# Performance work log

Hardware: AMD Instinct MI355X
Metric: run time of the kernel (lower is better)

## Reference

```python
import jax, jax.numpy as jnp
import numpy as np

B, Q, D, H, P, F = 16, 300, 256, 8, 4, 2048
HG = WG = 100          # feature-map height/width (hw = 10000, perfect square)
HW = HG * WG
DH = D // H
EPS = 1e-5


def _ln(x, g, b):
    m = x.mean(-1, keepdims=True)
    v = jnp.var(x, axis=-1, keepdims=True)
    return (x - m) * jax.lax.rsqrt(v + EPS) * g + b


def setup_inputs() -> dict:
    key = jax.random.key(0)
    ks = jax.random.split(key, 24)
    rn = lambda k, shape, s=0.02: jax.random.normal(k, shape, jnp.float32) * s
    return {
        "tgt": jax.random.normal(ks[0], (B, Q, D), jnp.float32),
        "memory": jax.random.normal(ks[1], (B, HW, D), jnp.float32),
        "in_proj_w": rn(ks[2], (D, 3 * D)), "in_proj_b": rn(ks[3], (3 * D,)),
        "out_proj_w": rn(ks[4], (D, D)), "out_proj_b": rn(ks[5], (D,)),
        "norm1_g": jnp.ones((D,), jnp.float32), "norm1_b": jnp.zeros((D,), jnp.float32),
        "ref_w": rn(ks[6], (D, 2)), "ref_b": rn(ks[7], (2,)),
        "off_w": rn(ks[8], (D, H * P * 2)), "off_b": rn(ks[9], (H * P * 2,)),
        "attw_w": rn(ks[10], (D, H * P)), "attw_b": rn(ks[11], (H * P,)),
        "vproj_w": rn(ks[12], (D, D)), "vproj_b": rn(ks[13], (D,)),
        "oproj_w": rn(ks[14], (D, D)), "oproj_b": rn(ks[15], (D,)),
        "norm2_g": jnp.ones((D,), jnp.float32), "norm2_b": jnp.zeros((D,), jnp.float32),
        "lin1_w": rn(ks[16], (D, F)), "lin1_b": rn(ks[17], (F,)),
        "lin2_w": rn(ks[18], (F, D)), "lin2_b": rn(ks[19], (D,)),
        "norm3_g": jnp.ones((D,), jnp.float32), "norm3_b": jnp.zeros((D,), jnp.float32),
    }


def reference(tgt, memory, in_proj_w, in_proj_b, out_proj_w, out_proj_b,
              norm1_g, norm1_b, ref_w, ref_b, off_w, off_b, attw_w, attw_b,
              vproj_w, vproj_b, oproj_w, oproj_b, norm2_g, norm2_b,
              lin1_w, lin1_b, lin2_w, lin2_b, norm3_g, norm3_b):
    # ---- self-attention (nn.MultiheadAttention, eval mode: dropout = identity)
    qkv = tgt @ in_proj_w + in_proj_b                      # [B,Q,3D]
    q, k, v = jnp.split(qkv, 3, axis=-1)
    q = q.reshape(B, Q, H, DH)
    k = k.reshape(B, Q, H, DH)
    v = v.reshape(B, Q, H, DH)
    scores = jnp.einsum('bqhd,bkhd->bhqk', q, k) / jnp.sqrt(jnp.float32(DH))
    attn = jax.nn.softmax(scores, axis=-1)
    sa = jnp.einsum('bhqk,bkhd->bqhd', attn, v).reshape(B, Q, D) @ out_proj_w + out_proj_b
    x = _ln(tgt + sa, norm1_g, norm1_b)

    # ---- reference points
    ref = jax.nn.sigmoid(x @ ref_w + ref_b)                # [B,Q,2] in (0,1)

    # ---- deformable cross-attention
    offs = (x @ off_w + off_b).reshape(B, Q, H, P, 2)
    wts = jax.nn.softmax((x @ attw_w + attw_b).reshape(B, Q, H, P), axis=-1)
    vals = (memory @ vproj_w + vproj_b).reshape(B, HW, H, DH)
    loc = jnp.clip(ref[:, :, None, None, :] + offs, 0.0, 1.0)
    sx = loc[..., 0] * (WG - 1)
    sy = loc[..., 1] * (HG - 1)
    x0 = jnp.floor(sx)
    y0 = jnp.floor(sy)
    x0i = jnp.clip(x0.astype(jnp.int32), 0, WG - 1)
    y0i = jnp.clip(y0.astype(jnp.int32), 0, HG - 1)
    x1i = jnp.clip(x0i + 1, 0, WG - 1)
    y1i = jnp.clip(y0i + 1, 0, HG - 1)
    wx1 = sx - x0
    wx0 = 1.0 - wx1
    wy1 = sy - y0
    wy0 = 1.0 - wy1
    bi = jnp.arange(B)[:, None, None, None]
    hi = jnp.arange(H)[None, None, :, None]

    def gather(yi, xi):                                    # [B,Q,H,P,DH]
        return vals[bi, yi * WG + xi, hi]

    samp = (gather(y0i, x0i) * (wx0 * wy0)[..., None]
            + gather(y1i, x0i) * (wx0 * wy1)[..., None]
            + gather(y0i, x1i) * (wx1 * wy0)[..., None]
            + gather(y1i, x1i) * (wx1 * wy1)[..., None])
    ca = (samp * wts[..., None]).sum(axis=3).reshape(B, Q, D) @ oproj_w + oproj_b
    x = _ln(x + ca, norm2_g, norm2_b)

    # ---- FFN
    ff = jax.nn.relu(x @ lin1_w + lin1_b) @ lin2_w + lin2_b
    return _ln(x + ff, norm3_g, norm3_b)
```

## Files before the change

### kernel.cpp

```cpp
#include <hip/hip_runtime.h>

#define NB   16
#define NQ   300
#define ND   256
#define NH   8
#define NP   4
#define NF   2048
#define NHW  10000
#define NWG  100
#define NROW 4800

typedef __attribute__((ext_vector_type(8))) short bf16x8;
typedef __attribute__((ext_vector_type(4))) float f32x4;

__device__ __forceinline__ unsigned short f2bf(float f) {
    unsigned u = __builtin_bit_cast(unsigned, f);
    u = (u + 0x7fffu + ((u >> 16) & 1u)) >> 16;
    return (unsigned short)u;
}
__device__ __forceinline__ float bf2f(unsigned short h) {
    unsigned u = ((unsigned)h) << 16;
    return __builtin_bit_cast(float, u);
}

__device__ __forceinline__ void gl_lds16(const unsigned short* g, unsigned short* l) {
    __builtin_amdgcn_global_load_lds(
        (__attribute__((address_space(1))) const void*)g,
        (__attribute__((address_space(3))) void*)l,
        16, 0, 0);
}

__global__ __launch_bounds__(256) void transpose_cast(
    const float* __restrict__ w_in,  const float* __restrict__ w_out,
    const float* __restrict__ w_vp,  const float* __restrict__ w_op,
    const float* __restrict__ w_l1,  const float* __restrict__ w_l2,
    unsigned short* __restrict__ o_in, unsigned short* __restrict__ o_out,
    unsigned short* __restrict__ o_vp, unsigned short* __restrict__ o_op,
    unsigned short* __restrict__ o_l1, unsigned short* __restrict__ o_l2)
{
    __shared__ float ts[64][65];
    int b = blockIdx.x;
    const float* src; unsigned short* dst; int K, N, ncx;
    if      (b < 48)  { src = w_in;  dst = o_in;  K = 256;  N = 768;  ncx = 12; }
    else if (b < 64)  { src = w_out; dst = o_out; K = 256;  N = 256;  ncx = 4;  b -= 48; }
    else if (b < 80)  { src = w_vp;  dst = o_vp;  K = 256;  N = 256;  ncx = 4;  b -= 64; }
    else if (b < 96)  { src = w_op;  dst = o_op;  K = 256;  N = 256;  ncx = 4;  b -= 80; }
    else if (b < 224) { src = w_l1;  dst = o_l1;  K = 256;  N = 2048; ncx = 32; b -= 96; }
    else              { src = w_l2;  dst = o_l2;  K = 2048; N = 256;  ncx = 4;  b -= 224; }
    const int n0 = (b % ncx) * 64, k0 = (b / ncx) * 64;
    const int t = threadIdx.x;
    const int r = t >> 4, c = t & 15;
    #pragma unroll
    for (int j = 0; j < 4; j++) {
        float4 v = *(const float4*)(src + (long)(k0 + j * 16 + r) * N + n0 + c * 4);
        ts[j * 16 + r][c * 4 + 0] = v.x;
        ts[j * 16 + r][c * 4 + 1] = v.y;
        ts[j * 16 + r][c * 4 + 2] = v.z;
        ts[j * 16 + r][c * 4 + 3] = v.w;
    }
    __syncthreads();
    #pragma unroll
    for (int j = 0; j < 4; j++) {
        unsigned short o[4];
        #pragma unroll
        for (int i = 0; i < 4; i++)
            o[i] = f2bf(ts[c * 4 + i][j * 16 + r]);
        *(uint2*)(dst + (long)(n0 + j * 16 + r) * K + k0 + c * 4) = *(uint2*)o;
    }
}

__global__ __launch_bounds__(256) void prep_head(
    const float* __restrict__ rw, const float* __restrict__ rb,
    const float* __restrict__ ow, const float* __restrict__ ob,
    const float* __restrict__ aw, const float* __restrict__ ab,
    unsigned short* __restrict__ o_hd, float* __restrict__ o_hb)
{
    int id = blockIdx.x * 256 + threadIdx.x;
    if (id < 32768) {
        int n = id >> 8, k = id & 255;
        float v;
        if (n < 2)       v = rw[k * 2 + n];
        else if (n < 66) v = ow[k * 64 + (n - 2)];
        else if (n < 98) v = aw[k * 32 + (n - 66)];
        else             v = 0.0f;
        o_hd[id] = f2bf(v);
        return;
    }
    id -= 32768;
    if (id < 128) {
        float v;
        if (id < 2)       v = rb[id];
        else if (id < 66) v = ob[id - 2];
        else if (id < 98) v = ab[id - 66];
        else              v = 0.0f;
        o_hb[id] = v;
    }
}

template <int RELU, int OUTBF, int SPLITK, int TM>
__global__ __launch_bounds__(256, 4) void gemm_bt(
    const float* __restrict__ A, const unsigned short* __restrict__ Bt,
    const float* __restrict__ bias, void* __restrict__ Cout,
    int M, int N, int K)
{
    static_assert(TM == 64, "tile is 64x128");
    __shared__ __align__(16) unsigned short As[2][64 * 32];
    __shared__ __align__(16) unsigned short Bs[2][128 * 32];
    const int t    = threadIdx.x;
    const long m0  = (long)blockIdx.y * 64;
    const int  n0  = blockIdx.x * 128;
    const int  wave = t >> 6, lane = t & 63;
    const int  l16 = lane & 15, quad = lane >> 4;
    const int  wm  = (wave >> 1) << 5;
    const int  wn  = (wave & 1) << 6;
    const int  fA  = (wave >> 1) << 1;
    const int  fB  = (wave & 1) << 2;

    f32x4 acc[2][4] = {};

    const int kChunk = K / SPLITK;
    const int kBeg   = (SPLITK > 1) ? blockIdx.z * kChunk : 0;
    const int nk     = kChunk / 32;

    const float* aP =
        A + (m0 + wave * 16 + l16) * (long)K + kBeg + (quad << 3);
    const unsigned short* bP =
        Bt + (long)(n0 + wave * 32 + l16) * K + kBeg + (quad << 3);
    unsigned short* aW  = &As[0][(wave << 9) + (lane << 3)];
    unsigned short* bW0 = &Bs[0][(wave << 10)];

    float4 fa0, fa1;
    auto loadA = [&](int kt) {
        fa0 = *(const float4*)(aP + kt * 32);
        fa1 = *(const float4*)(aP + kt * 32 + 4);
    };
    auto issueB = [&](int kt, int buf) {
        gl_lds16(bP + kt * 32,          bW0 + buf * 4096);
        gl_lds16(bP + kt * 32 + 16 * K, bW0 + buf * 4096 + 512);
    };
    auto writeA = [&](int buf) {
        unsigned short ta[8] = {f2bf(fa0.x), f2bf(fa0.y), f2bf(fa0.z), f2bf(fa0.w),
                                f2bf(fa1.x), f2bf(fa1.y), f2bf(fa1.z), f2bf(fa1.w)};
        *(uint4*)(aW + buf * 2048) = *(const uint4*)ta;
    };

    loadA(0);
    issueB(0, 0);
    writeA(0);
    __syncthreads();

    for (int kt = 0; kt < nk; kt++) {
        const int cur = kt & 1;
        if (kt + 1 < nk) {
            issueB(kt + 1, cur ^ 1);
            loadA(kt + 1);
        }

        const bf16x8 af0 = *(const bf16x8*)&As[cur][(fA + 0) * 512 + (lane << 3)];
        const bf16x8 af1 = *(const bf16x8*)&As[cur][(fA + 1) * 512 + (lane << 3)];
        #pragma unroll
        for (int j = 0; j < 4; j++) {
            const bf16x8 bv = *(const bf16x8*)&Bs[cur][(fB + j) * 512 + (lane << 3)];
            acc[0][j] = __builtin_amdgcn_mfma_f32_16x16x32_bf16(bv, af0, acc[0][j], 0, 0, 0);
            acc[1][j] = __builtin_amdgcn_mfma_f32_16x16x32_bf16(bv, af1, acc[1][j], 0, 0, 0);
        }

        if (kt + 1 < nk) {
            writeA(cur ^ 1);
            __syncthreads();
        }
    }

    float4 bj[4];
    #pragma unroll
    for (int j = 0; j < 4; j++)
        bj[j] = *(const float4*)&bias[n0 + wn + j * 16 + (quad << 2)];

    float* outp = (float*)Cout;
    float bscale = 1.0f;
    if (SPLITK > 1) {
        outp += (size_t)blockIdx.z * M * N;
        bscale = (blockIdx.z == 0) ? 1.0f : 0.0f;
    }

    #pragma unroll
    for (int i = 0; i < 2; i++) {
        const long gr = m0 + wm + i * 16 + l16;
        #pragma unroll
        for (int j = 0; j < 4; j++) {
            float4 v;
            v.x = acc[i][j][0] + bscale * bj[j].x;
            v.y = acc[i][j][1] + bscale * bj[j].y;
            v.z = acc[i][j][2] + bscale * bj[j].z;
            v.w = acc[i][j][3] + bscale * bj[j].w;
            if (RELU) {
                v.x = fmaxf(v.x, 0.f); v.y = fmaxf(v.y, 0.f);
                v.z = fmaxf(v.z, 0.f); v.w = fmaxf(v.w, 0.f);
            }
            const int gc = n0 + wn + j * 16 + (quad << 2);
            if (OUTBF) {
                unsigned short o[4] = {f2bf(v.x), f2bf(v.y), f2bf(v.z), f2bf(v.w)};
                *(uint2*)((unsigned short*)Cout + gr * N + gc) = *(uint2*)o;
            } else {
                *(float4*)(outp + gr * N + gc) = v;
            }
        }
    }
}

__global__ __launch_bounds__(256) void attn_kernel(
    const float* __restrict__ qkv, float* __restrict__ sa)
{
    __shared__ union {
        struct {
            unsigned short Ks[304][40];
            unsigned short Qs[64][40];
        } s;
        unsigned short Ps[4][16][328];
    } u;
    __shared__ unsigned short Vt[32][328];

    const int bh = blockIdx.y;
    const int b  = bh >> 3, h = bh & 7;
    const int q0 = blockIdx.x * 64;
    const int t  = threadIdx.x;

    for (int idx = t; idx < 304 * 8; idx += 256) {
        const int r = idx >> 3, c4 = (idx & 7) << 2;
        if (r < NQ) {
            const float4 kv = *(const float4*)(qkv + ((long)(b * NQ + r)) * 768 + 256 + h * 32 + c4);
            u.s.Ks[r][c4 + 0] = f2bf(kv.x); u.s.Ks[r][c4 + 1] = f2bf(kv.y);
            u.s.Ks[r][c4 + 2] = f2bf(kv.z); u.s.Ks[r][c4 + 3] = f2bf(kv.w);
        } else {
            u.s.Ks[r][c4 + 0] = 0; u.s.Ks[r][c4 + 1] = 0;
            u.s.Ks[r][c4 + 2] = 0; u.s.Ks[r][c4 + 3] = 0;
        }
    }
    for (int idx = t; idx < NQ * 8; idx += 256) {
        const int key = idx >> 3, dq = (idx & 7) << 2;
        const float4 vv = *(const float4*)(qkv + ((long)(b * NQ + key)) * 768 + 512 + h * 32 + dq);
        Vt[dq + 0][key] = f2bf(vv.x); Vt[dq + 1][key] = f2bf(vv.y);
        Vt[dq + 2][key] = f2bf(vv.z); Vt[dq + 3][key] = f2bf(vv.w);
    }
    for (int idx = t; idx < 32 * 20; idx += 256)
        Vt[idx / 20][300 + idx % 20] = 0;
    for (int idx = t; idx < 64 * 8; idx += 256) {
        const int r = idx >> 3, c4 = (idx & 7) << 2;
        const int q = q0 + r;
        if (q < NQ) {
            const float4 qv = *(const float4*)(qkv + ((long)(b * NQ + q)) * 768 + h * 32 + c4);
            u.s.Qs[r][c4 + 0] = f2bf(qv.x); u.s.Qs[r][c4 + 1] = f2bf(qv.y);
            u.s.Qs[r][c4 + 2] = f2bf(qv.z); u.s.Qs[r][c4 + 3] = f2bf(qv.w);
        } else {
            u.s.Qs[r][c4 + 0] = 0; u.s.Qs[r][c4 + 1] = 0;
            u.s.Qs[r][c4 + 2] = 0; u.s.Qs[r][c4 + 3] = 0;
        }
    }
    __syncthreads();

    const int wave = t >> 6, lane = t & 63;
    const int l16 = lane & 15, quad = lane >> 4;
    const float scale = 0.1767766952966369f;

    const bf16x8 aq = *(const bf16x8*)&u.s.Qs[wave * 16 + l16][quad * 8];
    f32x4 sacc[19];
    #pragma unroll
    for (int kt = 0; kt < 19; kt++) {
        const bf16x8 bk = *(const bf16x8*)&u.s.Ks[kt * 16 + l16][quad * 8];
        sacc[kt] = __builtin_amdgcn_mfma_f32_16x16x32_bf16(
            aq, bk, (f32x4){0.f, 0.f, 0.f, 0.f}, 0, 0, 0);
    }

    float inv[4];
    #pragma unroll
    for (int r = 0; r < 4; r++) {
        float m = -1e30f;
        #pragma unroll
        for (int kt = 0; kt < 19; kt++) {
            float s = sacc[kt][r] * scale;
            if (kt == 18 && l16 >= 12) s = -1e30f;
            sacc[kt][r] = s;
            m = fmaxf(m, s);
        }
        m = fmaxf(m, __shfl_xor(m, 1)); m = fmaxf(m, __shfl_xor(m, 2));
        m = fmaxf(m, __shfl_xor(m, 4)); m = fmaxf(m, __shfl_xor(m, 8));
        float sum = 0.f;
        #pragma unroll
        for (int kt = 0; kt < 19; kt++) {
            float p = __expf(sacc[kt][r] - m);
            sacc[kt][r] = p;
            sum += p;
        }
        sum += __shfl_xor(sum, 1); sum += __shfl_xor(sum, 2);
        sum += __shfl_xor(sum, 4); sum += __shfl_xor(sum, 8);
        inv[r] = 1.0f / sum;
    }

    __syncthreads();

    #pragma unroll
    for (int kt = 0; kt < 19; kt++)
        #pragma unroll
        for (int r = 0; r < 4; r++)
            u.Ps[wave][quad * 4 + r][kt * 16 + l16] = f2bf(sacc[kt][r] * inv[r]);
    #pragma unroll
    for (int r = 0; r < 4; r++)
        u.Ps[wave][quad * 4 + r][304 + l16] = 0;

    f32x4 o0 = {0.f, 0.f, 0.f, 0.f}, o1 = {0.f, 0.f, 0.f, 0.f};
    #pragma unroll
    for (int kt = 0; kt < 10; kt++) {
        const bf16x8 ap  = *(const bf16x8*)&u.Ps[wave][l16][kt * 32 + quad * 8];
        const bf16x8 bv0 = *(const bf16x8*)&Vt[l16][kt * 32 + quad * 8];
        const bf16x8 bv1 = *(const bf16x8*)&Vt[16 + l16][kt * 32 + quad * 8];
        o0 = __builtin_amdgcn_mfma_f32_16x16x32_bf16(ap, bv0, o0, 0, 0, 0);
        o1 = __builtin_amdgcn_mfma_f32_16x16x32_bf16(ap, bv1, o1, 0, 0, 0);
    }

    #pragma unroll
    for (int r = 0; r < 4; r++) {
        const int q = q0 + wave * 16 + quad * 4 + r;
        if (q < NQ) {
            float* op = sa + ((long)(b * NQ + q)) * ND + h * 32;
            op[l16]      = o0[r];
            op[16 + l16] = o1[r];
        }
    }
}

template <int NPART>
__global__ __launch_bounds__(256) void residual_ln(
    const float* __restrict__ a, const float* __restrict__ r,
    const float* __restrict__ gam, const float* __restrict__ bet,
    float* __restrict__ out, long pstride)
{
    const int row  = blockIdx.x * 4 + (threadIdx.x >> 6);
    const int lane = threadIdx.x & 63;
    const long base = (long)row * ND + lane * 4;
    float4 av = *(const float4*)(a + base);
    float4 rv = *(const float4*)(r + base);
    #pragma unroll
    for (int z = 1; z < NPART; z++) {
        float4 pv = *(const float4*)(r + z * pstride + base);
        rv.x += pv.x; rv.y += pv.y; rv.z += pv.z; rv.w += pv.w;
    }
    float x0 = av.x + rv.x, x1 = av.y + rv.y, x2 = av.z + rv.z, x3 = av.w + rv.w;
    float s  = x0 + x1 + x2 + x3;
    float s2 = x0 * x0 + x1 * x1 + x2 * x2 + x3 * x3;
    #pragma unroll
    for (int off = 32; off >= 1; off >>= 1) {
        s  += __shfl_xor(s, off);
        s2 += __shfl_xor(s2, off);
    }
    float mean = s * 0.00390625f;
    float var  = s2 * 0.00390625f - mean * mean;
    float rstd = rsqrtf(var + 1e-5f);
    float4 gv = *(const float4*)(gam + lane * 4);
    float4 bv = *(const float4*)(bet + lane * 4);
    float4 o;
    o.x = (x0 - mean) * rstd * gv.x + bv.x;
    o.y = (x1 - mean) * rstd * gv.y + bv.y;
    o.z = (x2 - mean) * rstd * gv.z + bv.z;
    o.w = (x3 - mean) * rstd * gv.w + bv.w;
    *(float4*)(out + base) = o;
}

__global__ __launch_bounds__(256) void meta_kernel(
    const float* __restrict__ res, float* __restrict__ meta)
{
    const int t   = threadIdx.x;
    const int row = blockIdx.x * 8 + (t >> 5);
    const int s   = t & 31;
    const int h   = s >> 2;
    const float* rp = res + (long)row * 128;
    const float rx = 1.f / (1.f + __expf(-rp[0]));
    const float ry = 1.f / (1.f + __expf(-rp[1]));
    const float offx = rp[2 + 2 * s], offy = rp[3 + 2 * s];
    const float a0 = rp[66 + h * 4 + 0], a1 = rp[66 + h * 4 + 1];
    const float a2 = rp[66 + h * 4 + 2], a3 = rp[66 + h * 4 + 3];
    const float mx = fmaxf(fmaxf(a0, a1), fmaxf(a2, a3));
    const float den = __expf(a0 - mx) + __expf(a1 - mx) +
                      __expf(a2 - mx) + __expf(a3 - mx);
    const float awt = __expf(rp[66 + s] - mx) / den;

    const float lx = fminf(fmaxf(rx + offx, 0.f), 1.f) * (NWG - 1);
    const float ly = fminf(fmaxf(ry + offy, 0.f), 1.f) * (NWG - 1);
    const float fx = floorf(lx), fy = floorf(ly);
    int x0 = (int)fx; x0 = min(max(x0, 0), NWG - 1);
    int y0 = (int)fy; y0 = min(max(y0, 0), NWG - 1);
    const int x1 = min(x0 + 1, NWG - 1);
    const int y1 = min(y0 + 1, NWG - 1);
    const float wx1 = lx - fx, wx0 = 1.f - wx1;
    const float wy1 = ly - fy, wy0 = 1.f - wy1;
    float4 m0, m1;
    m0.x = __int_as_float(y0 * NWG + x0);
    m0.y = __int_as_float(y0 * NWG + x1);
    m0.z = __int_as_float(y1 * NWG + x0);
    m0.w = __int_as_float(y1 * NWG + x1);
    m1.x = awt * wx0 * wy0;
    m1.y = awt * wx1 * wy0;
    m1.z = awt * wx0 * wy1;
    m1.w = awt * wx1 * wy1;
    float* mp = meta + (long)row * 256 + s * 8;
    *(float4*)mp       = m0;
    *(float4*)(mp + 4) = m1;
}

__global__ __launch_bounds__(256) void deform_gather(
    const float* __restrict__ meta, const unsigned short* __restrict__ vals,
    float* __restrict__ ca)
{
    const int row = blockIdx.x;
    const int b = row / NQ;
    __shared__ float ms[256];
    const int t = threadIdx.x;
    ms[t] = meta[(long)row * 256 + t];
    __syncthreads();
    const int h = t >> 5, d = t & 31;
    const unsigned short* vb = vals + (long)b * NHW * ND + h * 32 + d;
    float acc = 0.f;
    #pragma unroll
    for (int p = 0; p < NP; p++) {
        const float* mp = ms + h * 32 + p * 8;
        const int i00 = __float_as_int(mp[0]);
        const int i01 = __float_as_int(mp[1]);
        const int i10 = __float_as_int(mp[2]);
        const int i11 = __float_as_int(mp[3]);
        acc += mp[4] * bf2f(vb[(long)i00 * ND]);
        acc += mp[5] * bf2f(vb[(long)i01 * ND]);
        acc += mp[6] * bf2f(vb[(long)i10 * ND]);
        acc += mp[7] * bf2f(vb[(long)i11 * ND]);
    }
    ca[(long)row * ND + t] = acc;
}

extern "C" void kernel_launch(void* const* d_in, const int* in_sizes, int n_in,
                              void* d_out, int out_size, void* d_ws, size_t ws_size,
                              hipStream_t stream)
{
    (void)in_sizes; (void)n_in; (void)out_size; (void)ws_size;
    const float* tgt   = (const float*)d_in[0];
    const float* mem   = (const float*)d_in[1];
    const float* inpw  = (const float*)d_in[2];
    const float* inpb  = (const float*)d_in[3];
    const float* outw  = (const float*)d_in[4];
    const float* outb  = (const float*)d_in[5];
    const float* n1g   = (const float*)d_in[6];
    const float* n1b   = (const float*)d_in[7];
    const float* refw  = (const float*)d_in[8];
    const float* refb  = (const float*)d_in[9];
    const float* offw  = (const float*)d_in[10];
    const float* offb  = (const float*)d_in[11];
    const float* attww = (const float*)d_in[12];
    const float* attwb = (const float*)d_in[13];
    const float* vpw   = (const float*)d_in[14];
    const float* vpb   = (const float*)d_in[15];
    const float* opw   = (const float*)d_in[16];
    const float* opb   = (const float*)d_in[17];
    const float* n2g   = (const float*)d_in[18];
    const float* n2b   = (const float*)d_in[19];
    const float* l1w   = (const float*)d_in[20];
    const float* l1b   = (const float*)d_in[21];
    const float* l2w   = (const float*)d_in[22];
    const float* l2b   = (const float*)d_in[23];
    const float* n3g   = (const float*)d_in[24];
    const float* n3b   = (const float*)d_in[25];
    float* out = (float*)d_out;

    char* p = (char*)d_ws;
    auto alloc = [&](size_t bytes) {
        char* r = p; p += (bytes + 255) & ~(size_t)255; return (void*)r;
    };
    unsigned short* wtIn   = (unsigned short*)alloc(768 * 256 * 2);
    unsigned short* wtOut  = (unsigned short*)alloc(256 * 256 * 2);
    unsigned short* wtVp   = (unsigned short*)alloc(256 * 256 * 2);
    unsigned short* wtOp   = (unsigned short*)alloc(256 * 256 * 2);
    unsigned short* wtL1   = (unsigned short*)alloc(2048 * 256 * 2);
    unsigned short* wtL2   = (unsigned short*)alloc(256 * 2048 * 2);
    unsigned short* wtHead = (unsigned short*)alloc(128 * 256 * 2);
    float*          headb  = (float*)alloc(128 * 4);
    float* qkv  = (float*)alloc((size_t)NROW * 768 * 4);
    float* sa   = (float*)alloc((size_t)NROW * ND * 4);
    float* x1   = (float*)alloc((size_t)NROW * ND * 4);
    float* x2   = (float*)alloc((size_t)NROW * ND * 4);
    float* tmp  = (float*)alloc((size_t)NROW * ND * 4 * 4);
    float* ca   = (float*)alloc((size_t)NROW * ND * 4);
    float* meta = (float*)alloc((size_t)NROW * 256 * 4);
    void* uni = alloc((size_t)NB * NHW * ND * 2);
    unsigned short* vals = (unsigned short*)uni;
    float* h1 = (float*)uni;
    float* res = qkv;

    transpose_cast<<<352, 256, 0, stream>>>(
        inpw, outw, vpw, opw, l1w, l2w,
        wtIn, wtOut, wtVp, wtOp, wtL1, wtL2);
    prep_head<<<129, 256, 0, stream>>>(refw, refb, offw, offb, attww, attwb,
                                       wtHead, headb);

    gemm_bt<0, 0, 1, 64><<<dim3(6, 75), 256, 0, stream>>>(tgt, wtIn, inpb, qkv,
                                                          NROW, 768, 256);
    gemm_bt<0, 1, 1, 64><<<dim3(2, 2500), 256, 0, stream>>>(mem, wtVp, vpb, vals,
                                                            NB * NHW, 256, 256);
    attn_kernel<<<dim3(5, 128), 256, 0, stream>>>(qkv, sa);
    gemm_bt<0, 0, 1, 64><<<dim3(2, 75), 256, 0, stream>>>(sa, wtOut, outb, tmp,
                                                          NROW, 256, 256);
    residual_ln<1><<<1200, 256, 0, stream>>>(tgt, tmp, n1g, n1b, x1, 0);
    gemm_bt<0, 0, 1, 64><<<dim3(1, 75), 256, 0, stream>>>(x1, wtHead, headb, res,
                                                          NROW, 128, 256);
    meta_kernel<<<600, 256, 0, stream>>>(res, meta);
    deform_gather<<<4800, 256, 0, stream>>>(meta, vals, ca);
    gemm_bt<0, 0, 1, 64><<<dim3(2, 75), 256, 0, stream>>>(ca, wtOp, opb, tmp,
                                                          NROW, 256, 256);
    residual_ln<1><<<1200, 256, 0, stream>>>(x1, tmp, n2g, n2b, x2, 0);
    gemm_bt<1, 0, 1, 64><<<dim3(16, 75), 256, 0, stream>>>(x2, wtL1, l1b, h1,
                                                           NROW, 2048, 256);
    gemm_bt<0, 0, 4, 64><<<dim3(2, 75, 4), 256, 0, stream>>>(h1, wtL2, l2b, tmp,
                                                             NROW, 256, 2048);
    residual_ln<4><<<1200, 256, 0, stream>>>(x2, tmp, n3g, n3b, out,
                                             (long)NROW * 256);
}
```

Measured before the change: 514.9 us.

## Drop LDS staging in GEMM; load fragments directly from global into registers

```diff
diff --git a/kernel.cpp b/kernel.cpp
--- a/kernel.cpp
+++ b/kernel.cpp
@@ -23,11 +23,14 @@
     return __builtin_bit_cast(float, u);
 }
 
-__device__ __forceinline__ void gl_lds16(const unsigned short* g, unsigned short* l) {
-    __builtin_amdgcn_global_load_lds(
-        (__attribute__((address_space(1))) const void*)g,
-        (__attribute__((address_space(3))) void*)l,
-        16, 0, 0);
+__device__ __forceinline__ bf16x8 cvt8(float4 lo, float4 hi) {
+    unsigned r0, r1, r2, r3;
+    asm("v_cvt_pk_bf16_f32 %0, %1, %2" : "=v"(r0) : "v"(lo.x), "v"(lo.y));
+    asm("v_cvt_pk_bf16_f32 %0, %1, %2" : "=v"(r1) : "v"(lo.z), "v"(lo.w));
+    asm("v_cvt_pk_bf16_f32 %0, %1, %2" : "=v"(r2) : "v"(hi.x), "v"(hi.y));
+    asm("v_cvt_pk_bf16_f32 %0, %1, %2" : "=v"(r3) : "v"(hi.z), "v"(hi.w));
+    uint4 u = {r0, r1, r2, r3};
+    return __builtin_bit_cast(bf16x8, u);
 }
 
 __global__ __launch_bounds__(256) void transpose_cast(
@@ -97,15 +100,12 @@
     }
 }
 
-template <int RELU, int OUTBF, int SPLITK, int TM>
+template <int RELU, int OUTBF, int SPLITK>
 __global__ __launch_bounds__(256, 4) void gemm_bt(
     const float* __restrict__ A, const unsigned short* __restrict__ Bt,
     const float* __restrict__ bias, void* __restrict__ Cout,
     int M, int N, int K)
 {
-    static_assert(TM == 64, "tile is 64x128");
-    __shared__ __align__(16) unsigned short As[2][64 * 32];
-    __shared__ __align__(16) unsigned short Bs[2][128 * 32];
     const int t    = threadIdx.x;
     const long m0  = (long)blockIdx.y * 64;
     const int  n0  = blockIdx.x * 128;
@@ -113,8 +113,6 @@
     const int  l16 = lane & 15, quad = lane >> 4;
     const int  wm  = (wave >> 1) << 5;
     const int  wn  = (wave & 1) << 6;
-    const int  fA  = (wave >> 1) << 1;
-    const int  fB  = (wave & 1) << 2;
 
     f32x4 acc[2][4] = {};
 
@@ -122,53 +120,45 @@
     const int kBeg   = (SPLITK > 1) ? blockIdx.z * kChunk : 0;
     const int nk     = kChunk / 32;
 
-    const float* aP =
-        A + (m0 + wave * 16 + l16) * (long)K + kBeg + (quad << 3);
-    const unsigned short* bP =
-        Bt + (long)(n0 + wave * 32 + l16) * K + kBeg + (quad << 3);
-    unsigned short* aW  = &As[0][(wave << 9) + (lane << 3)];
-    unsigned short* bW0 = &Bs[0][(wave << 10)];
-
-    float4 fa0, fa1;
-    auto loadA = [&](int kt) {
-        fa0 = *(const float4*)(aP + kt * 32);
-        fa1 = *(const float4*)(aP + kt * 32 + 4);
+    const float* aP0 = A + (m0 + wm + l16) * (long)K + kBeg + (quad << 3);
+    const float* aP1 = aP0 + 16 * (long)K;
+    const unsigned short* bP = Bt + (long)(n0 + wn + l16) * K + kBeg + (quad << 3);
+    const long bStep = 16 * (long)K;
+
+    float4 xa0, xa1, xa2, xa3;
+    float4 ya0, ya1, ya2, ya3;
+
+    auto loadAX = [&](int kt) {
+        const int ko = kt << 5;
+        xa0 = *(const float4*)(aP0 + ko);     xa1 = *(const float4*)(aP0 + ko + 4);
+        xa2 = *(const float4*)(aP1 + ko);     xa3 = *(const float4*)(aP1 + ko + 4);
     };
-    auto issueB = [&](int kt, int buf) {
-        gl_lds16(bP + kt * 32,          bW0 + buf * 4096);
-        gl_lds16(bP + kt * 32 + 16 * K, bW0 + buf * 4096 + 512);
+    auto loadAY = [&](int kt) {
+        const int ko = kt << 5;
+        ya0 = *(const float4*)(aP0 + ko);     ya1 = *(const float4*)(aP0 + ko + 4);
+        ya2 = *(const float4*)(aP1 + ko);     ya3 = *(const float4*)(aP1 + ko + 4);
     };
-    auto writeA = [&](int buf) {
-        unsigned short ta[8] = {f2bf(fa0.x), f2bf(fa0.y), f2bf(fa0.z), f2bf(fa0.w),
-                                f2bf(fa1.x), f2bf(fa1.y), f2bf(fa1.z), f2bf(fa1.w)};
-        *(uint4*)(aW + buf * 2048) = *(const uint4*)ta;
+    auto compute = [&](float4 a0, float4 a1, float4 a2, float4 a3, int kt) {
+        const int ko = kt << 5;
+        bf16x8 bfr[4];
+        #pragma unroll
+        for (int j = 0; j < 4; j++)
+            bfr[j] = *(const bf16x8*)(bP + j * bStep + ko);
+        const bf16x8 af0 = cvt8(a0, a1);
+        const bf16x8 af1 = cvt8(a2, a3);
+        #pragma unroll
+        for (int j = 0; j < 4; j++) {
+            acc[0][j] = __builtin_amdgcn_mfma_f32_16x16x32_bf16(bfr[j], af0, acc[0][j], 0, 0, 0);
+            acc[1][j] = __builtin_amdgcn_mfma_f32_16x16x32_bf16(bfr[j], af1, acc[1][j], 0, 0, 0);
+        }
     };
 
-    loadA(0);
-    issueB(0, 0);
-    writeA(0);
-    __syncthreads();
-
-    for (int kt = 0; kt < nk; kt++) {
-        const int cur = kt & 1;
-        if (kt + 1 < nk) {
-            issueB(kt + 1, cur ^ 1);
-            loadA(kt + 1);
-        }
-
-        const bf16x8 af0 = *(const bf16x8*)&As[cur][(fA + 0) * 512 + (lane << 3)];
-        const bf16x8 af1 = *(const bf16x8*)&As[cur][(fA + 1) * 512 + (lane << 3)];
-        #pragma unroll
-        for (int j = 0; j < 4; j++) {
-            const bf16x8 bv = *(const bf16x8*)&Bs[cur][(fB + j) * 512 + (lane << 3)];
-            acc[0][j] = __builtin_amdgcn_mfma_f32_16x16x32_bf16(bv, af0, acc[0][j], 0, 0, 0);
-            acc[1][j] = __builtin_amdgcn_mfma_f32_16x16x32_bf16(bv, af1, acc[1][j], 0, 0, 0);
-        }
-
-        if (kt + 1 < nk) {
-            writeA(cur ^ 1);
-            __syncthreads();
-        }
+    loadAX(0);
+    for (int kt = 0; kt < nk; kt += 2) {
+        loadAY(kt + 1);
+        compute(xa0, xa1, xa2, xa3, kt);
+        if (kt + 2 < nk) loadAX(kt + 2);
+        compute(ya0, ya1, ya2, ya3, kt + 1);
     }
 
     float4 bj[4];
@@ -497,25 +487,25 @@
     prep_head<<<129, 256, 0, stream>>>(refw, refb, offw, offb, attww, attwb,
                                        wtHead, headb);
 
-    gemm_bt<0, 0, 1, 64><<<dim3(6, 75), 256, 0, stream>>>(tgt, wtIn, inpb, qkv,
-                                                          NROW, 768, 256);
-    gemm_bt<0, 1, 1, 64><<<dim3(2, 2500), 256, 0, stream>>>(mem, wtVp, vpb, vals,
-                                                            NB * NHW, 256, 256);
+    gemm_bt<0, 0, 1><<<dim3(6, 75), 256, 0, stream>>>(tgt, wtIn, inpb, qkv,
+                                                      NROW, 768, 256);
+    gemm_bt<0, 1, 1><<<dim3(2, 2500), 256, 0, stream>>>(mem, wtVp, vpb, vals,
+                                                        NB * NHW, 256, 256);
     attn_kernel<<<dim3(5, 128), 256, 0, stream>>>(qkv, sa);
-    gemm_bt<0, 0, 1, 64><<<dim3(2, 75), 256, 0, stream>>>(sa, wtOut, outb, tmp,
-                                                          NROW, 256, 256);
+    gemm_bt<0, 0, 1><<<dim3(2, 75), 256, 0, stream>>>(sa, wtOut, outb, tmp,
+                                                      NROW, 256, 256);
     residual_ln<1><<<1200, 256, 0, stream>>>(tgt, tmp, n1g, n1b, x1, 0);
-    gemm_bt<0, 0, 1, 64><<<dim3(1, 75), 256, 0, stream>>>(x1, wtHead, headb, res,
-                                                          NROW, 128, 256);
+    gemm_bt<0, 0, 1><<<dim3(1, 75), 256, 0, stream>>>(x1, wtHead, headb, res,
+                                                      NROW, 128, 256);
     meta_kernel<<<600, 256, 0, stream>>>(res, meta);
     deform_gather<<<4800, 256, 0, stream>>>(meta, vals, ca);
-    gemm_bt<0, 0, 1, 64><<<dim3(2, 75), 256, 0, stream>>>(ca, wtOp, opb, tmp,
-                                                          NROW, 256, 256);
+    gemm_bt<0, 0, 1><<<dim3(2, 75), 256, 0, stream>>>(ca, wtOp, opb, tmp,
+                                                      NROW, 256, 256);
     residual_ln<1><<<1200, 256, 0, stream>>>(x1, tmp, n2g, n2b, x2, 0);
-    gemm_bt<1, 0, 1, 64><<<dim3(16, 75), 256, 0, stream>>>(x2, wtL1, l1b, h1,
-                                                           NROW, 2048, 256);
-    gemm_bt<0, 0, 4, 64><<<dim3(2, 75, 4), 256, 0, stream>>>(h1, wtL2, l2b, tmp,
-                                                             NROW, 256, 2048);
+    gemm_bt<1, 0, 1><<<dim3(16, 75), 256, 0, stream>>>(x2, wtL1, l1b, h1,
+                                                       NROW, 2048, 256);
+    gemm_bt<0, 0, 4><<<dim3(2, 75, 4), 256, 0, stream>>>(h1, wtL2, l2b, tmp,
+                                                         NROW, 256, 2048);
     residual_ln<4><<<1200, 256, 0, stream>>>(x2, tmp, n3g, n3b, out,
                                              (long)NROW * 256);
 }
```

New measurement: 627.4 us. +21.9%, slower.

## Enlarge GEMM tiles to 128xTN with 512-thread blocks and packed bf16 convert

Applied to the files above, without the earlier changes.

```diff
diff --git a/kernel.cpp b/kernel.cpp
--- a/kernel.cpp
+++ b/kernel.cpp
@@ -21,6 +21,16 @@
 __device__ __forceinline__ float bf2f(unsigned short h) {
     unsigned u = ((unsigned)h) << 16;
     return __builtin_bit_cast(float, u);
+}
+
+__device__ __forceinline__ bf16x8 cvt8(float4 lo, float4 hi) {
+    unsigned r0, r1, r2, r3;
+    asm("v_cvt_pk_bf16_f32 %0, %1, %2" : "=v"(r0) : "v"(lo.x), "v"(lo.y));
+    asm("v_cvt_pk_bf16_f32 %0, %1, %2" : "=v"(r1) : "v"(lo.z), "v"(lo.w));
+    asm("v_cvt_pk_bf16_f32 %0, %1, %2" : "=v"(r2) : "v"(hi.x), "v"(hi.y));
+    asm("v_cvt_pk_bf16_f32 %0, %1, %2" : "=v"(r3) : "v"(hi.z), "v"(hi.w));
+    uint4 u = {r0, r1, r2, r3};
+    return __builtin_bit_cast(bf16x8, u);
 }
 
 __device__ __forceinline__ void gl_lds16(const unsigned short* g, unsigned short* l) {
@@ -97,55 +107,75 @@
     }
 }
 
-template <int RELU, int OUTBF, int SPLITK, int TM>
-__global__ __launch_bounds__(256, 4) void gemm_bt(
+template <int RELU, int OUTBF, int SPLITK, int TN>
+__global__ __launch_bounds__(512, 4) void gemm_bt(
     const float* __restrict__ A, const unsigned short* __restrict__ Bt,
     const float* __restrict__ bias, void* __restrict__ Cout,
     int M, int N, int K)
 {
-    static_assert(TM == 64, "tile is 64x128");
-    __shared__ __align__(16) unsigned short As[2][64 * 32];
-    __shared__ __align__(16) unsigned short Bs[2][128 * 32];
+    constexpr int NFB = TN / 16;
+    constexpr int WN  = TN / 64;
+    constexpr int AI  = WN;
+
+    __shared__ __align__(16) unsigned short As[2][8 * 512];
+    __shared__ __align__(16) unsigned short Bs[2][NFB * 512];
+
     const int t    = threadIdx.x;
-    const long m0  = (long)blockIdx.y * 64;
-    const int  n0  = blockIdx.x * 128;
+    const long m0  = (long)blockIdx.y * 128;
+    const int  n0  = blockIdx.x * TN;
     const int  wave = t >> 6, lane = t & 63;
     const int  l16 = lane & 15, quad = lane >> 4;
-    const int  wm  = (wave >> 1) << 5;
-    const int  wn  = (wave & 1) << 6;
-    const int  fA  = (wave >> 1) << 1;
-    const int  fB  = (wave & 1) << 2;
-
-    f32x4 acc[2][4] = {};
+    const int  wmi = wave / WN, wni = wave % WN;
+    const int  wm  = wmi * (AI * 16);
+    const int  wn  = wni * 64;
+    const int  fA  = wmi * AI;
+    const int  fB  = wni * 4;
+
+    f32x4 acc[AI][4] = {};
 
     const int kChunk = K / SPLITK;
     const int kBeg   = (SPLITK > 1) ? blockIdx.z * kChunk : 0;
     const int nk     = kChunk / 32;
 
-    const float* aP =
-        A + (m0 + wave * 16 + l16) * (long)K + kBeg + (quad << 3);
-    const unsigned short* bP =
-        Bt + (long)(n0 + wave * 32 + l16) * K + kBeg + (quad << 3);
-    unsigned short* aW  = &As[0][(wave << 9) + (lane << 3)];
-    unsigned short* bW0 = &Bs[0][(wave << 10)];
-
-    float4 fa0, fa1;
+    const long aRow   = m0 + wave * 16 + l16;
+    const bool aValid = (aRow < M);
+    const float* aP   = A + aRow * (long)K + kBeg + (quad << 3);
+    unsigned short* aW = &As[0][(wave << 9) + (lane << 3)];
+
+    const unsigned short* bP;
+    unsigned short* bW;
+    if constexpr (TN == 256) {
+        bP = Bt + (long)(n0 + wave * 32 + l16) * K + kBeg + (quad << 3);
+        bW = &Bs[0][wave << 10];
+    } else {
+        bP = Bt + (long)(n0 + wave * 16 + l16) * K + kBeg + (quad << 3);
+        bW = &Bs[0][wave << 9];
+    }
+
+    float4 la0 = make_float4(0.f, 0.f, 0.f, 0.f);
+    float4 la1 = make_float4(0.f, 0.f, 0.f, 0.f);
+
     auto loadA = [&](int kt) {
-        fa0 = *(const float4*)(aP + kt * 32);
-        fa1 = *(const float4*)(aP + kt * 32 + 4);
+        if (aValid) {
+            la0 = *(const float4*)(aP + kt * 32);
+            la1 = *(const float4*)(aP + kt * 32 + 4);
+        }
+    };
+    auto writeA = [&](int buf) {
+        const bf16x8 v = cvt8(la0, la1);
+        *(bf16x8*)(aW + buf * 4096) = v;
     };
     auto issueB = [&](int kt, int buf) {
-        gl_lds16(bP + kt * 32,          bW0 + buf * 4096);
-        gl_lds16(bP + kt * 32 + 16 * K, bW0 + buf * 4096 + 512);
+        if constexpr (TN == 256) {
+            gl_lds16(bP + kt * 32,          bW + buf * (NFB * 512));
+            gl_lds16(bP + kt * 32 + 16 * (long)K, bW + buf * (NFB * 512) + 512);
+        } else {
+            gl_lds16(bP + kt * 32,          bW + buf * (NFB * 512));
+        }
     };
-    auto writeA = [&](int buf) {
-        unsigned short ta[8] = {f2bf(fa0.x), f2bf(fa0.y), f2bf(fa0.z), f2bf(fa0.w),
-                                f2bf(fa1.x), f2bf(fa1.y), f2bf(fa1.z), f2bf(fa1.w)};
-        *(uint4*)(aW + buf * 2048) = *(const uint4*)ta;
-    };
-
+
+    issueB(0, 0);
     loadA(0);
-    issueB(0, 0);
     writeA(0);
     __syncthreads();
 
@@ -156,14 +186,19 @@
             loadA(kt + 1);
         }
 
-        const bf16x8 af0 = *(const bf16x8*)&As[cur][(fA + 0) * 512 + (lane << 3)];
-        const bf16x8 af1 = *(const bf16x8*)&As[cur][(fA + 1) * 512 + (lane << 3)];
-        #pragma unroll
-        for (int j = 0; j < 4; j++) {
-            const bf16x8 bv = *(const bf16x8*)&Bs[cur][(fB + j) * 512 + (lane << 3)];
-            acc[0][j] = __builtin_amdgcn_mfma_f32_16x16x32_bf16(bv, af0, acc[0][j], 0, 0, 0);
-            acc[1][j] = __builtin_amdgcn_mfma_f32_16x16x32_bf16(bv, af1, acc[1][j], 0, 0, 0);
-        }
+        bf16x8 af[AI], bfr[4];
+        #pragma unroll
+        for (int i = 0; i < AI; i++)
+            af[i] = *(const bf16x8*)&As[cur][(fA + i) * 512 + (lane << 3)];
+        #pragma unroll
+        for (int j = 0; j < 4; j++)
+            bfr[j] = *(const bf16x8*)&Bs[cur][(fB + j) * 512 + (lane << 3)];
+        #pragma unroll
+        for (int i = 0; i < AI; i++)
+            #pragma unroll
+            for (int j = 0; j < 4; j++)
+                acc[i][j] = __builtin_amdgcn_mfma_f32_16x16x32_bf16(
+                    bfr[j], af[i], acc[i][j], 0, 0, 0);
 
         if (kt + 1 < nk) {
             writeA(cur ^ 1);
@@ -184,25 +219,27 @@
     }
 
     #pragma unroll
-    for (int i = 0; i < 2; i++) {
+    for (int i = 0; i < AI; i++) {
         const long gr = m0 + wm + i * 16 + l16;
-        #pragma unroll
-        for (int j = 0; j < 4; j++) {
-            float4 v;
-            v.x = acc[i][j][0] + bscale * bj[j].x;
-            v.y = acc[i][j][1] + bscale * bj[j].y;
-            v.z = acc[i][j][2] + bscale * bj[j].z;
-            v.w = acc[i][j][3] + bscale * bj[j].w;
-            if (RELU) {
-                v.x = fmaxf(v.x, 0.f); v.y = fmaxf(v.y, 0.f);
-                v.z = fmaxf(v.z, 0.f); v.w = fmaxf(v.w, 0.f);
-            }
-            const int gc = n0 + wn + j * 16 + (quad << 2);
-            if (OUTBF) {
-                unsigned short o[4] = {f2bf(v.x), f2bf(v.y), f2bf(v.z), f2bf(v.w)};
-                *(uint2*)((unsigned short*)Cout + gr * N + gc) = *(uint2*)o;
-            } else {
-                *(float4*)(outp + gr * N + gc) = v;
+        if (gr < M) {
+            #pragma unroll
+            for (int j = 0; j < 4; j++) {
+                float4 v;
+                v.x = acc[i][j][0] + bscale * bj[j].x;
+                v.y = acc[i][j][1] + bscale * bj[j].y;
+                v.z = acc[i][j][2] + bscale * bj[j].z;
+                v.w = acc[i][j][3] + bscale * bj[j].w;
+                if (RELU) {
+                    v.x = fmaxf(v.x, 0.f); v.y = fmaxf(v.y, 0.f);
+                    v.z = fmaxf(v.z, 0.f); v.w = fmaxf(v.w, 0.f);
+                }
+                const int gc = n0 + wn + j * 16 + (quad << 2);
+                if (OUTBF) {
+                    unsigned short o[4] = {f2bf(v.x), f2bf(v.y), f2bf(v.z), f2bf(v.w)};
+                    *(uint2*)((unsigned short*)Cout + gr * N + gc) = *(uint2*)o;
+                } else {
+                    *(float4*)(outp + gr * N + gc) = v;
+                }
             }
         }
     }
@@ -497,25 +534,25 @@
     prep_head<<<129, 256, 0, stream>>>(refw, refb, offw, offb, attww, attwb,
                                        wtHead, headb);
 
-    gemm_bt<0, 0, 1, 64><<<dim3(6, 75), 256, 0, stream>>>(tgt, wtIn, inpb, qkv,
-                                                          NROW, 768, 256);
-    gemm_bt<0, 1, 1, 64><<<dim3(2, 2500), 256, 0, stream>>>(mem, wtVp, vpb, vals,
-                                                            NB * NHW, 256, 256);
+    gemm_bt<0, 0, 1, 256><<<dim3(3, 38), 512, 0, stream>>>(tgt, wtIn, inpb, qkv,
+                                                           NROW, 768, 256);
+    gemm_bt<0, 1, 1, 256><<<dim3(1, 1250), 512, 0, stream>>>(mem, wtVp, vpb, vals,
+                                                             NB * NHW, 256, 256);
     attn_kernel<<<dim3(5, 128), 256, 0, stream>>>(qkv, sa);
-    gemm_bt<0, 0, 1, 64><<<dim3(2, 75), 256, 0, stream>>>(sa, wtOut, outb, tmp,
-                                                          NROW, 256, 256);
+    gemm_bt<0, 0, 1, 256><<<dim3(1, 38), 512, 0, stream>>>(sa, wtOut, outb, tmp,
+                                                           NROW, 256, 256);
     residual_ln<1><<<1200, 256, 0, stream>>>(tgt, tmp, n1g, n1b, x1, 0);
-    gemm_bt<0, 0, 1, 64><<<dim3(1, 75), 256, 0, stream>>>(x1, wtHead, headb, res,
-                                                          NROW, 128, 256);
+    gemm_bt<0, 0, 1, 128><<<dim3(1, 38), 512, 0, stream>>>(x1, wtHead, headb, res,
+                                                           NROW, 128, 256);
     meta_kernel<<<600, 256, 0, stream>>>(res, meta);
     deform_gather<<<4800, 256, 0, stream>>>(meta, vals, ca);
-    gemm_bt<0, 0, 1, 64><<<dim3(2, 75), 256, 0, stream>>>(ca, wtOp, opb, tmp,
-                                                          NROW, 256, 256);
+    gemm_bt<0, 0, 1, 256><<<dim3(1, 38), 512, 0, stream>>>(ca, wtOp, opb, tmp,
+                                                           NROW, 256, 256);
     residual_ln<1><<<1200, 256, 0, stream>>>(x1, tmp, n2g, n2b, x2, 0);
-    gemm_bt<1, 0, 1, 64><<<dim3(16, 75), 256, 0, stream>>>(x2, wtL1, l1b, h1,
+    gemm_bt<1, 0, 1, 256><<<dim3(8, 38), 512, 0, stream>>>(x2, wtL1, l1b, h1,
                                                            NROW, 2048, 256);
-    gemm_bt<0, 0, 4, 64><<<dim3(2, 75, 4), 256, 0, stream>>>(h1, wtL2, l2b, tmp,
-                                                             NROW, 256, 2048);
+    gemm_bt<0, 0, 4, 256><<<dim3(1, 38, 4), 512, 0, stream>>>(h1, wtL2, l2b, tmp,
+                                                              NROW, 256, 2048);
     residual_ln<4><<<1200, 256, 0, stream>>>(x2, tmp, n3g, n3b, out,
                                              (long)NROW * 256);
 }
```

Result: faster. 499.0 us (-3.1%).
